# Kernel tuning notes

Measured on AMD Instinct MI355X. Metric: run time of the kernel, lower is better.

The kernel has to match this reference:

```python
import jax, jax.numpy as jnp
import numpy as np

N, D, H, E = 32768, 1024, 1024, 4


def setup_inputs() -> dict:
    key = jax.random.key(0)
    ks = jax.random.split(key, 10)
    s = 0.02  # xavier-ish init scale for stability
    return {
        "features": jax.random.normal(ks[0], (N, D), dtype=jnp.float32),
        "symbol_ids": jax.random.randint(ks[1], (N,), 0, E, dtype=jnp.int32),
        "W1": jax.random.normal(ks[2], (E, D, H), dtype=jnp.float32) * s,
        "b1": jax.random.normal(ks[3], (E, H), dtype=jnp.float32) * s,
        "W2": jax.random.normal(ks[4], (E, H, H), dtype=jnp.float32) * s,
        "b2": jax.random.normal(ks[5], (E, H), dtype=jnp.float32) * s,
        "W3": jax.random.normal(ks[6], (E, H, 1), dtype=jnp.float32) * s,
        "b3": jax.random.normal(ks[7], (E, 1), dtype=jnp.float32) * s,
        "slope": jax.random.normal(ks[8], (E,), dtype=jnp.float32),
        "intercept": jax.random.normal(ks[9], (E,), dtype=jnp.float32),
    }


def reference(features, symbol_ids, W1, b1, W2, b2, W3, b3, slope, intercept):
    # Run every atom through every expert MLP (E is tiny), then select by symbol.
    # h1: [E, N, H]
    h = jax.nn.relu(jnp.einsum("nd,edh->enh", features, W1) + b1[:, None, :])
    h = jax.nn.relu(jnp.einsum("enh,ehk->enk", h, W2) + b2[:, None, :])
    y = (jnp.einsum("enk,eko->eno", h, W3) + b3[:, None, :])[..., 0]  # [E, N]
    per_atom = slope[:, None] * y + intercept[:, None]                # [E, N]
    sel = symbol_ids[None, :] == jnp.arange(E, dtype=symbol_ids.dtype)[:, None]
    atomic_energies = jnp.sum(jnp.where(sel, per_atom, 0.0), axis=0)  # [N]
    image_energy = jnp.sum(atomic_energies)                           # scalar
    return image_energy
```

## Files before the change

kernel.cpp:

```cpp
#include <hip/hip_runtime.h>
#include <hip/hip_bf16.h>
#include <stdint.h>

#define NATOMS 32768
#define DDIM   1024
#define HDIM   1024
#define ENUM   4
#define MCAP   33792

typedef unsigned short u16;
typedef unsigned char  u8;
typedef __attribute__((ext_vector_type(8)))  int   i32x8;
typedef __attribute__((ext_vector_type(16))) float f32x16;

static const size_t XP_OFF   = 0;
static const size_t H1_OFF   = XP_OFF  + (size_t)MCAP * 1024;
static const size_t W1T_OFF  = H1_OFF  + (size_t)MCAP * 1024;
static const size_t W2T_OFF  = W1T_OFF + (size_t)ENUM * 1024 * 1024;
static const size_t PERM_OFF = W2T_OFF + (size_t)ENUM * 1024 * 1024;
static const size_t META_OFF = PERM_OFF + (size_t)MCAP * 4;

__device__ __forceinline__ u8 f2fp8(float x) {
    int w = __builtin_amdgcn_cvt_pk_fp8_f32(x, x, 0, false);
    return (u8)(w & 0xFF);
}

__global__ void k_count(const int* __restrict__ sym, int* __restrict__ meta) {
    __shared__ int cnt[4];
    int t = threadIdx.x;
    if (t < 4) cnt[t] = 0;
    __syncthreads();
    int n = blockIdx.x * 256 + t;
    int lane = t & 63;
    int e = sym[n];
#pragma unroll
    for (int j = 0; j < ENUM; ++j) {
        unsigned long long mask = __ballot(e == j);
        if (mask) {
            int leader = __ffsll((long long)mask) - 1;
            if (lane == leader) atomicAdd(&cnt[j], __popcll(mask));
        }
    }
    __syncthreads();
    if (t < 4) meta[256 + blockIdx.x * 4 + t] = cnt[t];
}

__global__ void k_offsets(int* __restrict__ meta, const float* __restrict__ slope,
                          const float* __restrict__ b3, const float* __restrict__ inter,
                          float* __restrict__ out, int* __restrict__ perm) {
    __shared__ int tot[4], padS[4], padE[4];
    int t = threadIdx.x;
    if (t < 4) {
        int s = 0;
#pragma unroll 8
        for (int b = 0; b < 128; ++b) s += meta[256 + b * 4 + t];
        tot[t] = s;
    }
    __syncthreads();
    if (t == 0) {
        int off = 0;
        float c = 0.f;
        for (int e = 0; e < 4; ++e) {
            int cnt = tot[e];
            meta[e * 16]     = cnt;
            meta[128 + e]    = off;
            meta[64 + e*16]  = off;
            padS[e] = off + cnt;
            c += (float)cnt * (slope[e] * b3[e] + inter[e]);
            off += (cnt + 255) & ~255;
            padE[e] = off;
        }
        meta[132] = off;
        out[0] = c;
    }
    __syncthreads();
#pragma unroll
    for (int e = 0; e < 4; ++e)
        for (int i = padS[e] + t; i < padE[e]; i += 256) perm[i] = 0;
}

__global__ void k_scatter(const int* __restrict__ sym, int* __restrict__ meta,
                          int* __restrict__ perm) {
    int n = blockIdx.x * 256 + threadIdx.x;
    int lane = threadIdx.x & 63;
    int e = sym[n];
#pragma unroll
    for (int j = 0; j < ENUM; ++j) {
        unsigned long long mask = __ballot(e == j);
        if (mask) {
            int leader = __ffsll((long long)mask) - 1;
            int base = 0;
            if (lane == leader)
                base = atomicAdd(&meta[64 + j * 16], __popcll(mask));
            base = __shfl(base, leader, 64);
            if (e == j) {
                int rank = __popcll(mask & ((1ull << lane) - 1ull));
                perm[base + rank] = n;
            }
        }
    }
}

__global__ void k_conv8(const float* __restrict__ F, u8* __restrict__ X8) {
    int g = blockIdx.x * 256 + threadIdx.x;
    const float* fp = F + (size_t)g * 8;
    int w0 = 0, w1 = 0;
    w0 = __builtin_amdgcn_cvt_pk_fp8_f32(fp[0], fp[1], w0, false);
    w0 = __builtin_amdgcn_cvt_pk_fp8_f32(fp[2], fp[3], w0, true);
    w1 = __builtin_amdgcn_cvt_pk_fp8_f32(fp[4], fp[5], w1, false);
    w1 = __builtin_amdgcn_cvt_pk_fp8_f32(fp[6], fp[7], w1, true);
    uint2 v; v.x = (unsigned)w0; v.y = (unsigned)w1;
    *(uint2*)(void*)(X8 + (size_t)g * 8) = v;
}

__global__ void k_transw(const float* __restrict__ W1, u8* __restrict__ W1T,
                         const float* __restrict__ W2, u8* __restrict__ W2T) {
    __shared__ u8 tile[64][65];
    const float* W  = blockIdx.z ? W2  : W1;
    u8*          WT = blockIdx.z ? W2T : W1T;
    int e  = blockIdx.y;
    int tn = blockIdx.x & 15;
    int tk = blockIdx.x >> 4;
    const float* Wp = W  + (size_t)e * 1024 * 1024;
    u8*         WTp = WT + (size_t)e * 1024 * 1024;
    int c = threadIdx.x & 63, r0 = threadIdx.x >> 6;
#pragma unroll
    for (int i = 0; i < 16; ++i) {
        int r = r0 + i * 4;
        tile[r][c] = f2fp8(32.0f * Wp[(size_t)(tk * 64 + r) * 1024 + tn * 64 + c]);
    }
    __syncthreads();
#pragma unroll
    for (int i = 0; i < 16; ++i) {
        int r = r0 + i * 4;
        WTp[(size_t)(tn * 64 + r) * 1024 + tk * 64 + c] = tile[c][r];
    }
}

template <bool FUSE, bool PERM>
__global__ __launch_bounds__(256, 2)
void k_gemm(const u8* __restrict__ A, const u8* __restrict__ BT,
            const float* __restrict__ bias, u8* __restrict__ C,
            const int* __restrict__ meta, const float* __restrict__ W3,
            const float* __restrict__ slope, float* __restrict__ out,
            const int* __restrict__ perm) {
    __shared__ u8 As[256 * 128];
    __shared__ u8 Bs[128 * 128];
    const int* offs = meta + 128;

    const int flat = blockIdx.y * 8 + blockIdx.x;
    const int wgid = (flat & 7) * 132 + (flat >> 3);
    const int mt = wgid >> 3;
    const int nt = wgid & 7;
    const int m0 = mt * 256, n0 = nt * 128;
    if (m0 >= meta[132]) return;
    const int e = (m0 >= offs[1]) + (m0 >= offs[2]) + (m0 >= offs[3]);

    const int t = threadIdx.x;
    const int w = t >> 6, lane = t & 63;
    const int l31 = lane & 31, khalf = lane >> 5;
    const int wm = w & 1, wn = w >> 1;

    const u8* Bg = BT + (size_t)e * 1024 * 1024 + (size_t)n0 * 1024;

    const int srow = t >> 3;
    const int gcol = (((t & 7) ^ (srow & 7) ^ ((srow >> 3) & 3)) * 16);

    const u8* arow[8];
#pragma unroll
    for (int i = 0; i < 8; ++i) {
        int r = i * 32 + srow;
        size_t src = PERM ? (size_t)perm[m0 + r] : (size_t)(m0 + r);
        arow[i] = A + src * 1024 + gcol;
    }
    const u8* brow[4];
#pragma unroll
    for (int i = 0; i < 4; ++i)
        brow[i] = Bg + (size_t)(i * 32 + srow) * 1024 + gcol;

    f32x16 acc[4][2] = {};

    for (int kt = 0; kt < 1024 / 128; ++kt) {
        const int kb = kt * 128;
#pragma unroll
        for (int i = 0; i < 8; ++i)
            __builtin_amdgcn_global_load_lds((const void*)(arow[i] + kb),
                (void*)(As + i * 4096 + w * 1024), 16, 0, 0);
#pragma unroll
        for (int i = 0; i < 4; ++i)
            __builtin_amdgcn_global_load_lds((const void*)(brow[i] + kb),
                (void*)(Bs + i * 4096 + w * 1024), 16, 0, 0);
        __syncthreads();

#pragma unroll
        for (int kk = 0; kk < 2; ++kk) {
            const int c0 = 4 * kk + 2 * khalf;
            i32x8 b[2];
#pragma unroll
            for (int ni = 0; ni < 2; ++ni) {
                int n = wn * 64 + ni * 32 + l31;
                const u8* base = Bs + n * 128;
                int sw = (n & 7) ^ ((n >> 3) & 3);
                int lo = ((c0 ^ sw) << 4);
                union { uint4 q[2]; i32x8 v; } u;
                u.q[0] = *(const uint4*)(const void*)(base + lo);
                u.q[1] = *(const uint4*)(const void*)(base + (lo ^ 16));
                b[ni] = u.v;
            }
#pragma unroll
            for (int mi = 0; mi < 4; ++mi) {
                int m = wm * 128 + mi * 32 + l31;
                const u8* base = As + m * 128;
                int sw = (m & 7) ^ ((m >> 3) & 3);
                int lo = ((c0 ^ sw) << 4);
                union { uint4 q[2]; i32x8 v; } u;
                u.q[0] = *(const uint4*)(const void*)(base + lo);
                u.q[1] = *(const uint4*)(const void*)(base + (lo ^ 16));
                i32x8 a = u.v;
#pragma unroll
                for (int ni = 0; ni < 2; ++ni)
                    acc[mi][ni] = __builtin_amdgcn_mfma_scale_f32_32x32x64_f8f6f4(
                        a, b[ni], acc[mi][ni],
                        0, 0,
                        0, 0x7F7F7F7F,
                        0, 0x7A7A7A7A);
            }
        }
        __syncthreads();
    }

    if (!FUSE) {
#pragma unroll
        for (int ni = 0; ni < 2; ++ni) {
            int col = n0 + wn * 64 + ni * 32 + l31;
            float bv = bias[e * 1024 + col];
#pragma unroll
            for (int mi = 0; mi < 4; ++mi) {
                int rowb = m0 + wm * 128 + mi * 32 + 4 * khalf;
#pragma unroll
                for (int reg = 0; reg < 16; ++reg) {
                    int rowg = rowb + (reg & 3) + 8 * (reg >> 2);
                    float v = acc[mi][ni][reg] + bv;
                    v = v > 0.f ? v : 0.f;
                    C[(size_t)rowg * 1024 + col] = f2fp8(v);
                }
            }
        }
    } else {
        const int segEnd = offs[e] + meta[e * 16];
        const float se = slope[e];
        float psum = 0.f;
#pragma unroll
        for (int ni = 0; ni < 2; ++ni) {
            int col = n0 + wn * 64 + ni * 32 + l31;
            float bv  = bias[e * 1024 + col];
            float w3s = W3[e * 1024 + col] * se;
#pragma unroll
            for (int mi = 0; mi < 4; ++mi) {
                int rowb = m0 + wm * 128 + mi * 32 + 4 * khalf;
#pragma unroll
                for (int reg = 0; reg < 16; ++reg) {
                    int rowg = rowb + (reg & 3) + 8 * (reg >> 2);
                    float v = acc[mi][ni][reg] + bv;
                    v = v > 0.f ? v : 0.f;
                    psum += (rowg < segEnd) ? v * w3s : 0.f;
                }
            }
        }
#pragma unroll
        for (int o = 32; o; o >>= 1) psum += __shfl_xor(psum, o, 64);
        float* red = (float*)As;
        if (lane == 0) red[w] = psum;
        __syncthreads();
        if (t == 0) atomicAdd(out, red[0] + red[1] + red[2] + red[3]);
    }
}

extern "C" void kernel_launch(void* const* d_in, const int* in_sizes, int n_in,
                              void* d_out, int out_size, void* d_ws, size_t ws_size,
                              hipStream_t stream) {
    const float* features = (const float*)d_in[0];
    const int*   sym      = (const int*)d_in[1];
    const float* W1       = (const float*)d_in[2];
    const float* b1       = (const float*)d_in[3];
    const float* W2       = (const float*)d_in[4];
    const float* b2       = (const float*)d_in[5];
    const float* W3       = (const float*)d_in[6];
    const float* b3       = (const float*)d_in[7];
    const float* slope    = (const float*)d_in[8];
    const float* inter    = (const float*)d_in[9];
    float* out = (float*)d_out;

    char* ws  = (char*)d_ws;
    u8*  X8   = (u8*)(ws + XP_OFF);
    u8*  H1b  = (u8*)(ws + H1_OFF);
    u8*  W1T  = (u8*)(ws + W1T_OFF);
    u8*  W2T  = (u8*)(ws + W2T_OFF);
    int* perm = (int*)(ws + PERM_OFF);
    int* meta = (int*)(ws + META_OFF);

    k_count<<<NATOMS / 256, 256, 0, stream>>>(sym, meta);
    k_offsets<<<1, 256, 0, stream>>>(meta, slope, b3, inter, out, perm);
    k_scatter<<<NATOMS / 256, 256, 0, stream>>>(sym, meta, perm);
    k_conv8<<<(NATOMS * 128) / 256, 256, 0, stream>>>(features, X8);
    k_transw<<<dim3(256, 4, 2), 256, 0, stream>>>(W1, W1T, W2, W2T);
    k_gemm<false, true><<<dim3(8, 132), 256, 0, stream>>>(X8, W1T, b1, H1b, meta,
                                                          nullptr, nullptr, nullptr,
                                                          perm);
    k_gemm<true, false><<<dim3(8, 132), 256, 0, stream>>>(H1b, W2T, b2, nullptr,
                                                          meta, W3, slope, out,
                                                          nullptr);
}
```

Before: 339.1 us.

## Double-buffer GEMM LDS tiles with 128x128 tiles and fuse prep kernels

The three routing kernels (count, offsets, scatter) are merged into one single-block prep kernel that uses shared-memory cursors, removing two launches and the global atomics. The FP8 GEMM drops from a 256x128 to a 128x128 M tile with twice as many workgroups, and double-buffers the A/B LDS tiles so the next k-tile's global-to-LDS loads overlap the current MFMAs, waiting with explicit vmcnt. The workgroup-to-tile mapping changes to a grouped raster. The trade-off is less B reuse per tile, a single-block serial prep over 32K atoms, and hand-written waitcnt/barrier logic that may be fragile.

New measurement: 373.4 us. +10.1%, slower.

```diff
diff --git a/kernel.cpp b/kernel.cpp
--- a/kernel.cpp
+++ b/kernel.cpp
@@ -25,79 +25,65 @@
     return (u8)(w & 0xFF);
 }
 
-__global__ void k_count(const int* __restrict__ sym, int* __restrict__ meta) {
-    __shared__ int cnt[4];
-    int t = threadIdx.x;
+__global__ __launch_bounds__(1024)
+void k_prep(const int* __restrict__ sym, int* __restrict__ meta,
+            int* __restrict__ perm, const float* __restrict__ slope,
+            const float* __restrict__ b3, const float* __restrict__ inter,
+            float* __restrict__ out) {
+    __shared__ int cnt[4], cur[4], offw[4], padE[4];
+    int t = threadIdx.x, lane = t & 63;
     if (t < 4) cnt[t] = 0;
     __syncthreads();
-    int n = blockIdx.x * 256 + t;
-    int lane = t & 63;
-    int e = sym[n];
-#pragma unroll
-    for (int j = 0; j < ENUM; ++j) {
-        unsigned long long mask = __ballot(e == j);
-        if (mask) {
-            int leader = __ffsll((long long)mask) - 1;
-            if (lane == leader) atomicAdd(&cnt[j], __popcll(mask));
-        }
-    }
-    __syncthreads();
-    if (t < 4) meta[256 + blockIdx.x * 4 + t] = cnt[t];
-}
-
-__global__ void k_offsets(int* __restrict__ meta, const float* __restrict__ slope,
-                          const float* __restrict__ b3, const float* __restrict__ inter,
-                          float* __restrict__ out, int* __restrict__ perm) {
-    __shared__ int tot[4], padS[4], padE[4];
-    int t = threadIdx.x;
-    if (t < 4) {
-        int s = 0;
-#pragma unroll 8
-        for (int b = 0; b < 128; ++b) s += meta[256 + b * 4 + t];
-        tot[t] = s;
+    for (int base = 0; base < NATOMS; base += 1024) {
+        int e = sym[base + t];
+#pragma unroll
+        for (int j = 0; j < ENUM; ++j) {
+            unsigned long long mask = __ballot(e == j);
+            if (mask && lane == __ffsll((long long)mask) - 1)
+                atomicAdd(&cnt[j], __popcll(mask));
+        }
     }
     __syncthreads();
     if (t == 0) {
         int off = 0;
         float c = 0.f;
         for (int e = 0; e < 4; ++e) {
-            int cnt = tot[e];
-            meta[e * 16]     = cnt;
-            meta[128 + e]    = off;
-            meta[64 + e*16]  = off;
-            padS[e] = off + cnt;
-            c += (float)cnt * (slope[e] * b3[e] + inter[e]);
-            off += (cnt + 255) & ~255;
+            int cc = cnt[e];
+            meta[e * 16]  = cc;
+            meta[128 + e] = off;
+            offw[e] = off;
+            cur[e]  = off;
+            c += (float)cc * (slope[e] * b3[e] + inter[e]);
+            off += (cc + 255) & ~255;
             padE[e] = off;
         }
         meta[132] = off;
         out[0] = c;
     }
     __syncthreads();
-#pragma unroll
-    for (int e = 0; e < 4; ++e)
-        for (int i = padS[e] + t; i < padE[e]; i += 256) perm[i] = 0;
-}
-
-__global__ void k_scatter(const int* __restrict__ sym, int* __restrict__ meta,
-                          int* __restrict__ perm) {
-    int n = blockIdx.x * 256 + threadIdx.x;
-    int lane = threadIdx.x & 63;
-    int e = sym[n];
-#pragma unroll
-    for (int j = 0; j < ENUM; ++j) {
-        unsigned long long mask = __ballot(e == j);
-        if (mask) {
-            int leader = __ffsll((long long)mask) - 1;
-            int base = 0;
-            if (lane == leader)
-                base = atomicAdd(&meta[64 + j * 16], __popcll(mask));
-            base = __shfl(base, leader, 64);
-            if (e == j) {
-                int rank = __popcll(mask & ((1ull << lane) - 1ull));
-                perm[base + rank] = n;
-            }
-        }
+    for (int base = 0; base < NATOMS; base += 1024) {
+        int n = base + t;
+        int e = sym[n];
+#pragma unroll
+        for (int j = 0; j < ENUM; ++j) {
+            unsigned long long mask = __ballot(e == j);
+            if (mask) {
+                int leader = __ffsll((long long)mask) - 1;
+                int b = 0;
+                if (lane == leader) b = atomicAdd(&cur[j], __popcll(mask));
+                b = __shfl(b, leader, 64);
+                if (e == j) {
+                    int rank = __popcll(mask & ((1ull << lane) - 1ull));
+                    perm[b + rank] = n;
+                }
+            }
+        }
+    }
+    __syncthreads();
+#pragma unroll
+    for (int e = 0; e < 4; ++e) {
+        int ps = offw[e] + cnt[e];
+        for (int i = ps + t; i < padE[e]; i += 1024) perm[i] = 0;
     }
 }
 
@@ -144,15 +130,14 @@
             const int* __restrict__ meta, const float* __restrict__ W3,
             const float* __restrict__ slope, float* __restrict__ out,
             const int* __restrict__ perm) {
-    __shared__ u8 As[256 * 128];
-    __shared__ u8 Bs[128 * 128];
+    __shared__ u8 As[2][128 * 128];
+    __shared__ u8 Bs[2][128 * 128];
     const int* offs = meta + 128;
 
     const int flat = blockIdx.y * 8 + blockIdx.x;
-    const int wgid = (flat & 7) * 132 + (flat >> 3);
-    const int mt = wgid >> 3;
-    const int nt = wgid & 7;
-    const int m0 = mt * 256, n0 = nt * 128;
+    const int mt = (flat >> 6) * 8 + (flat & 7);
+    const int nt = (flat & 63) >> 3;
+    const int m0 = mt * 128, n0 = nt * 128;
     if (m0 >= meta[132]) return;
     const int e = (m0 >= offs[1]) + (m0 >= offs[2]) + (m0 >= offs[3]);
 
@@ -166,9 +151,9 @@
     const int srow = t >> 3;
     const int gcol = (((t & 7) ^ (srow & 7) ^ ((srow >> 3) & 3)) * 16);
 
-    const u8* arow[8];
-#pragma unroll
-    for (int i = 0; i < 8; ++i) {
+    const u8* arow[4];
+#pragma unroll
+    for (int i = 0; i < 4; ++i) {
         int r = i * 32 + srow;
         size_t src = PERM ? (size_t)perm[m0 + r] : (size_t)(m0 + r);
         arow[i] = A + src * 1024 + gcol;
@@ -178,20 +163,39 @@
     for (int i = 0; i < 4; ++i)
         brow[i] = Bg + (size_t)(i * 32 + srow) * 1024 + gcol;
 
-    f32x16 acc[4][2] = {};
-
-    for (int kt = 0; kt < 1024 / 128; ++kt) {
-        const int kb = kt * 128;
-#pragma unroll
-        for (int i = 0; i < 8; ++i)
-            __builtin_amdgcn_global_load_lds((const void*)(arow[i] + kb),
-                (void*)(As + i * 4096 + w * 1024), 16, 0, 0);
-#pragma unroll
-        for (int i = 0; i < 4; ++i)
-            __builtin_amdgcn_global_load_lds((const void*)(brow[i] + kb),
-                (void*)(Bs + i * 4096 + w * 1024), 16, 0, 0);
-        __syncthreads();
-
+    f32x16 acc[2][2] = {};
+
+#define SSTAGE(buf, ktile)                                                      \
+    do {                                                                        \
+        const size_t kb_ = (size_t)(ktile) * 128;                               \
+        _Pragma("unroll")                                                       \
+        for (int i = 0; i < 4; ++i)                                             \
+            __builtin_amdgcn_global_load_lds((const void*)(arow[i] + kb_),      \
+                (void*)(&As[buf][i * 4096 + w * 1024]), 16, 0, 0);              \
+        _Pragma("unroll")                                                       \
+        for (int i = 0; i < 4; ++i)                                             \
+            __builtin_amdgcn_global_load_lds((const void*)(brow[i] + kb_),      \
+                (void*)(&Bs[buf][i * 4096 + w * 1024]), 16, 0, 0);              \
+    } while (0)
+#define FENCE asm volatile("" ::: "memory")
+#define BAR   do { FENCE; __builtin_amdgcn_s_barrier(); FENCE; } while (0)
+
+    SSTAGE(0, 0);
+
+#pragma unroll 2
+    for (int kt = 0; kt < 8; ++kt) {
+        const int cur = kt & 1;
+        BAR;
+        if (kt < 7) {
+            SSTAGE(cur ^ 1, kt + 1);
+            asm volatile("s_waitcnt vmcnt(8)" ::: "memory");
+        } else {
+            asm volatile("s_waitcnt vmcnt(0)" ::: "memory");
+        }
+        BAR;
+
+        const u8* Ab = &As[cur][0];
+        const u8* Bb = &Bs[cur][0];
 #pragma unroll
         for (int kk = 0; kk < 2; ++kk) {
             const int c0 = 4 * kk + 2 * khalf;
@@ -199,7 +203,7 @@
 #pragma unroll
             for (int ni = 0; ni < 2; ++ni) {
                 int n = wn * 64 + ni * 32 + l31;
-                const u8* base = Bs + n * 128;
+                const u8* base = Bb + n * 128;
                 int sw = (n & 7) ^ ((n >> 3) & 3);
                 int lo = ((c0 ^ sw) << 4);
                 union { uint4 q[2]; i32x8 v; } u;
@@ -208,9 +212,9 @@
                 b[ni] = u.v;
             }
 #pragma unroll
-            for (int mi = 0; mi < 4; ++mi) {
-                int m = wm * 128 + mi * 32 + l31;
-                const u8* base = As + m * 128;
+            for (int mi = 0; mi < 2; ++mi) {
+                int m = wm * 64 + mi * 32 + l31;
+                const u8* base = Ab + m * 128;
                 int sw = (m & 7) ^ ((m >> 3) & 3);
                 int lo = ((c0 ^ sw) << 4);
                 union { uint4 q[2]; i32x8 v; } u;
@@ -226,8 +230,10 @@
                         0, 0x7A7A7A7A);
             }
         }
-        __syncthreads();
-    }
+    }
+#undef SSTAGE
+#undef FENCE
+#undef BAR
 
     if (!FUSE) {
 #pragma unroll
@@ -235,8 +241,8 @@
             int col = n0 + wn * 64 + ni * 32 + l31;
             float bv = bias[e * 1024 + col];
 #pragma unroll
-            for (int mi = 0; mi < 4; ++mi) {
-                int rowb = m0 + wm * 128 + mi * 32 + 4 * khalf;
+            for (int mi = 0; mi < 2; ++mi) {
+                int rowb = m0 + wm * 64 + mi * 32 + 4 * khalf;
 #pragma unroll
                 for (int reg = 0; reg < 16; ++reg) {
                     int rowg = rowb + (reg & 3) + 8 * (reg >> 2);
@@ -256,8 +262,8 @@
             float bv  = bias[e * 1024 + col];
             float w3s = W3[e * 1024 + col] * se;
 #pragma unroll
-            for (int mi = 0; mi < 4; ++mi) {
-                int rowb = m0 + wm * 128 + mi * 32 + 4 * khalf;
+            for (int mi = 0; mi < 2; ++mi) {
+                int rowb = m0 + wm * 64 + mi * 32 + 4 * khalf;
 #pragma unroll
                 for (int reg = 0; reg < 16; ++reg) {
                     int rowg = rowb + (reg & 3) + 8 * (reg >> 2);
@@ -269,7 +275,8 @@
         }
 #pragma unroll
         for (int o = 32; o; o >>= 1) psum += __shfl_xor(psum, o, 64);
-        float* red = (float*)As;
+        __syncthreads();
+        float* red = (float*)&As[0][0];
         if (lane == 0) red[w] = psum;
         __syncthreads();
         if (t == 0) atomicAdd(out, red[0] + red[1] + red[2] + red[3]);
@@ -299,15 +306,13 @@
     int* perm = (int*)(ws + PERM_OFF);
     int* meta = (int*)(ws + META_OFF);
 
-    k_count<<<NATOMS / 256, 256, 0, stream>>>(sym, meta);
-    k_offsets<<<1, 256, 0, stream>>>(meta, slope, b3, inter, out, perm);
-    k_scatter<<<NATOMS / 256, 256, 0, stream>>>(sym, meta, perm);
+    k_prep<<<1, 1024, 0, stream>>>(sym, meta, perm, slope, b3, inter, out);
     k_conv8<<<(NATOMS * 128) / 256, 256, 0, stream>>>(features, X8);
     k_transw<<<dim3(256, 4, 2), 256, 0, stream>>>(W1, W1T, W2, W2T);
-    k_gemm<false, true><<<dim3(8, 132), 256, 0, stream>>>(X8, W1T, b1, H1b, meta,
+    k_gemm<false, true><<<dim3(8, 264), 256, 0, stream>>>(X8, W1T, b1, H1b, meta,
                                                           nullptr, nullptr, nullptr,
                                                           perm);
-    k_gemm<true, false><<<dim3(8, 132), 256, 0, stream>>>(H1b, W2T, b2, nullptr,
+    k_gemm<true, false><<<dim3(8, 264), 256, 0, stream>>>(H1b, W2T, b2, nullptr,
                                                           meta, W3, slope, out,
                                                           nullptr);
 }
```
